# Optimization experiments

Measured on AMD Instinct MI355X. Metric: run time of the kernel, lower is better.

The kernel has to match this reference:

```python
import jax, jax.numpy as jnp
import numpy as np

N, E, DIM = 50000, 1_600_000, 96
H = DIM // 3      # num_heads = dim/3 = 32
HD = 3            # head_dim = dim/num_heads = 3
SCALE = 2.0
EPS = 1e-5


def ln(x, g, b):
    mu = x.mean(-1, keepdims=True)
    var = ((x - mu) ** 2).mean(-1, keepdims=True)
    return (x - mu) * jax.lax.rsqrt(var + EPS) * g + b


def setup_inputs() -> dict:
    key = jax.random.key(0)
    ks = jax.random.split(key, 40)
    rn = lambda k, shp, s=0.05: jax.random.normal(k, shp, jnp.float32) * s
    inp = {
        'feat': jax.random.normal(ks[0], (N, DIM), jnp.float32),
        'edge': jax.random.normal(ks[1], (E, H), jnp.float32),
        'Wq': rn(ks[2], (DIM, DIM)), 'bq': jnp.zeros((DIM,), jnp.float32),
        'Wk': rn(ks[3], (DIM, DIM)), 'bk': jnp.zeros((DIM,), jnp.float32),
        'Wv': rn(ks[4], (DIM, DIM)), 'bv': jnp.zeros((DIM,), jnp.float32),
        'We': rn(ks[5], (H, H)), 'be': jnp.zeros((H,), jnp.float32),
        'Wb': rn(ks[6], (H, H)), 'bb': jnp.zeros((H,), jnp.float32),
        'Wvv': rn(ks[7], (DIM + H, DIM)), 'bvv': jnp.zeros((DIM,), jnp.float32),
        'Wf0': rn(ks[8], (H, 2 * H)), 'bf0': jnp.zeros((2 * H,), jnp.float32),
        'Wf1': rn(ks[9], (2 * H, H)), 'bf1': jnp.zeros((H,), jnp.float32),
        'Wm0': rn(ks[10], (DIM, 2 * DIM)), 'bm0': jnp.zeros((2 * DIM,), jnp.float32),
        'Wm1': rn(ks[11], (2 * DIM, DIM)), 'bm1': jnp.zeros((DIM,), jnp.float32),
        'g_n0': jnp.ones((DIM,), jnp.float32), 'b_n0': jnp.zeros((DIM,), jnp.float32),
        'g_e0': jnp.ones((H,), jnp.float32), 'b_e0': jnp.zeros((H,), jnp.float32),
        'g_e1': jnp.ones((H,), jnp.float32), 'b_e1': jnp.zeros((H,), jnp.float32),
        'g_m': jnp.ones((DIM,), jnp.float32), 'b_m': jnp.zeros((DIM,), jnp.float32),
        'w': jnp.zeros((1,), jnp.float32),
        'src': jax.random.randint(ks[12], (E,), 0, N),
        'dst': jax.random.randint(ks[13], (E,), 0, N),
    }
    return inp


def reference(feat, edge, Wq, bq, Wk, bk, Wv, bv, We, be, Wb, bb, Wvv, bvv,
              Wf0, bf0, Wf1, bf1, Wm0, bm0, Wm1, bm1,
              g_n0, b_n0, g_e0, b_e0, g_e1, b_e1, g_m, b_m, w, src, dst):
    n = feat.shape[0]
    h0 = ln(feat, g_n0, b_n0)            # [N, DIM]
    ew = ln(edge, g_e0, b_e0)            # [E, H]
    q = (h0 @ Wq + bq).reshape(n, H, HD)
    k = (h0 @ Wk + bk).reshape(n, H, HD)
    v = (h0 @ Wv + bv).reshape(n, H, HD)
    ve = (ew @ We + be)[:, :, None]       # [E, H, 1]
    B = ew @ Wb + bb                      # [E, H]
    # src_dot_dst('k','q'): (k[src] * q[dst]).sum(-1)
    score = jnp.sum(k[src] * q[dst], axis=-1) / SCALE + B   # [E, H]
    e = score + edge                       # [E, H]
    se = jnp.concatenate([v[src], ve], axis=-1)              # [E, H, 4]
    # edge_softmax: softmax over incoming edges of each dst node, per head
    m = jax.ops.segment_max(score, dst, num_segments=n)      # [N, H]
    ex = jnp.exp(score - m[dst])
    den = jax.ops.segment_sum(ex, dst, num_segments=n)
    att = (ex / den[dst])[:, :, None]                        # [E, H, 1]
    agg = jax.ops.segment_sum(att * se, dst, num_segments=n) # [N, H, 4]
    h = feat * (1.0 + w) + (agg.reshape(n, -1) @ Wvv + bvv)  # [N, DIM]
    # up_expert Mlp (pre-LN residual)
    hn = ln(h, g_m, b_m)
    h = h + (jax.nn.relu(hn @ Wm0 + bm0) @ Wm1 + bm1)
    # edge FFN residual
    en = ln(e, g_e1, b_e1)
    e = e + (jax.nn.relu(en @ Wf0 + bf0) @ Wf1 + bf1)
    return h, e
```

## Files before the change

### kernel.cpp

```cpp
#include <hip/hip_runtime.h>
#include <cstdint>
#include <cstddef>


typedef short  s16x8 __attribute__((ext_vector_type(8)));
typedef short  s16x4 __attribute__((ext_vector_type(4)));
typedef float  f32x4 __attribute__((ext_vector_type(4)));

__device__ __forceinline__ unsigned short f2b(float x) {
    union { float f; unsigned u; } v; v.f = x;
    unsigned r = v.u + 0x7FFF + ((v.u >> 16) & 1);
    return (unsigned short)(r >> 16);
}
__device__ __forceinline__ float b2f(unsigned short u) {
    union { unsigned u; float f; } v; v.u = ((unsigned)u) << 16; return v.f;
}

template<int MULTI, int LNA, int A16, int RELU, int RES>
__global__ __launch_bounds__(256) void mgemm_kernel(
    const void* __restrict__ Av, int lda,
    const float* __restrict__ B0, const float* __restrict__ B1,
    const float* __restrict__ B2, int ldb,
    const float* __restrict__ bias0, const float* __restrict__ bias1,
    const float* __restrict__ bias2,
    const float* __restrict__ lng, const float* __restrict__ lnbv,
    const float* __restrict__ resid, const float* __restrict__ wptr,
    float* __restrict__ C, int ldc, unsigned short* __restrict__ C16,
    int M, int K)
{
    __shared__ unsigned short sAL[64 * 200];
    __shared__ unsigned short sB[96 * 40];

    const int tid = threadIdx.x;
    const int m0 = blockIdx.x * 64;
    const int y  = blockIdx.y;
    const float* B = MULTI ? (y == 0 ? B0 : (y == 1 ? B1 : B2)) : B0;
    const int nbB = MULTI ? 0 : y * 96;
    const int nbC = y * 96;
    const int w = tid >> 6, l = tid & 63, fr = l & 15, kg = l >> 4;
    const int KP = K + 8;

    if (LNA) {
        const float* Af = (const float*)Av;
        const int row = 16 * w + fr;
        const int grow = m0 + row;
        float x[24];
        if (grow < M) {
            #pragma unroll
            for (int t = 0; t < 6; t++)
                *(float4*)&x[t * 4] = *(const float4*)(Af + (size_t)grow * lda + 24 * kg + t * 4);
        } else {
            #pragma unroll
            for (int t = 0; t < 24; t++) x[t] = 0.f;
        }
        float s = 0.f;
        #pragma unroll
        for (int t = 0; t < 24; t++) s += x[t];
        s += __shfl_xor(s, 16, 64); s += __shfl_xor(s, 32, 64);
        float mu = s * (1.f / 96.f);
        float v2 = 0.f;
        #pragma unroll
        for (int t = 0; t < 24; t++) { float d = x[t] - mu; v2 += d * d; }
        v2 += __shfl_xor(v2, 16, 64); v2 += __shfl_xor(v2, 32, 64);
        float rs = rsqrtf(v2 * (1.f / 96.f) + 1e-5f);
        #pragma unroll
        for (int t3 = 0; t3 < 3; t3++) {
            s16x8 yv;
            #pragma unroll
            for (int u = 0; u < 8; u++) {
                int cidx = 24 * kg + t3 * 8 + u;
                yv[u] = (short)f2b((x[t3 * 8 + u] - mu) * rs * lng[cidx] + lnbv[cidx]);
            }
            *(s16x8*)&sAL[row * KP + 24 * kg + t3 * 8] = yv;
        }
    } else {
        const int nseg = K >> 3;
        for (int idx = tid; idx < 64 * nseg; idx += 256) {
            int row = idx / nseg, k8 = (idx - row * nseg) * 8;
            int grow = m0 + row;
            s16x8 a8 = (s16x8){0, 0, 0, 0, 0, 0, 0, 0};
            if (grow < M) {
                if (A16) {
                    a8 = *(const s16x8*)((const unsigned short*)Av + (size_t)grow * lda + k8);
                } else {
                    const float* Af = (const float*)Av;
                    float4 v0 = *(const float4*)(Af + (size_t)grow * lda + k8);
                    float4 v1 = *(const float4*)(Af + (size_t)grow * lda + k8 + 4);
                    a8[0] = (short)f2b(v0.x); a8[1] = (short)f2b(v0.y);
                    a8[2] = (short)f2b(v0.z); a8[3] = (short)f2b(v0.w);
                    a8[4] = (short)f2b(v1.x); a8[5] = (short)f2b(v1.y);
                    a8[6] = (short)f2b(v1.z); a8[7] = (short)f2b(v1.w);
                }
            }
            *(s16x8*)&sAL[row * KP + k8] = a8;
        }
    }

    f32x4 acc[6];
    #pragma unroll
    for (int i = 0; i < 6; i++) acc[i] = (f32x4){0.f, 0.f, 0.f, 0.f};

    for (int kc = 0; kc < K; kc += 32) {
        #pragma unroll
        for (int r = 0; r < 3; r++) {
            int idx = tid + 256 * r;
            int k = idx / 24, n4 = (idx - k * 24) * 4;
            float4 v = *(const float4*)(B + (size_t)(kc + k) * ldb + nbB + n4);
            sB[(n4 + 0) * 40 + k] = f2b(v.x);
            sB[(n4 + 1) * 40 + k] = f2b(v.y);
            sB[(n4 + 2) * 40 + k] = f2b(v.z);
            sB[(n4 + 3) * 40 + k] = f2b(v.w);
        }
        __syncthreads();
        {
            s16x8 a = *(s16x8*)&sAL[(16 * w + fr) * KP + kc + kg * 8];
            #pragma unroll
            for (int nt = 0; nt < 6; nt++) {
                s16x8 b = *(s16x8*)&sB[(16 * nt + fr) * 40 + kg * 8];
                acc[nt] = __builtin_amdgcn_mfma_f32_16x16x32_bf16(a, b, acc[nt], 0, 0, 0);
            }
        }
        __syncthreads();
    }

    float scale = 1.f;
    if (RES) scale = wptr ? (1.f + wptr[0]) : 1.f;
    const float* biasp = MULTI ? (y == 0 ? bias0 : (y == 1 ? bias1 : bias2)) : bias0;
    const int bbase = MULTI ? 0 : nbB;

    #pragma unroll
    for (int nt = 0; nt < 6; nt++) {
        int cl = nt * 16 + fr;
        float bv = biasp[bbase + cl];
        int gcol = nbC + cl;
        #pragma unroll
        for (int r = 0; r < 4; r++) {
            int row = m0 + 16 * w + 4 * kg + r;
            if (row >= M) continue;
            float v = acc[nt][r] + bv;
            if (RELU) v = fmaxf(v, 0.f);
            if (MULTI) {
                C16[(size_t)row * 288 + gcol] = f2b(v);
            } else {
                if (RES) v += scale * resid[(size_t)row * ldc + gcol];
                C[(size_t)row * ldc + gcol] = v;
            }
        }
    }
}

__global__ __launch_bounds__(256) void prep_kernel(
    const float* __restrict__ Wb, const float* __restrict__ We,
    const float* __restrict__ Wf0, const float* __restrict__ Wf1,
    unsigned short* __restrict__ WbWe16, unsigned short* __restrict__ Wf0T16,
    unsigned short* __restrict__ Wf1T16)
{
    const int t = threadIdx.x;
    for (int i = t; i < 2048; i += 256) {
        int n = i >> 5, k = i & 31;
        float v = (n < 32) ? Wb[k * 32 + n] : We[k * 32 + (n - 32)];
        WbWe16[i] = f2b(v);
    }
    for (int i = t; i < 2048; i += 256) {
        int n = i >> 5, k = i & 31;
        Wf0T16[i] = f2b(Wf0[k * 64 + n]);
    }
    for (int i = t; i < 2048; i += 256) {
        int n = i >> 6, k = i & 63;
        Wf1T16[i] = f2b(Wf1[k * 32 + n]);
    }
}

__global__ __launch_bounds__(256) void count_kernel(
    const int* __restrict__ dst, int* __restrict__ cnt,
    int* __restrict__ rank, int E)
{
    int i = blockIdx.x * 256 + threadIdx.x;
    if (i < E) rank[i] = atomicAdd(&cnt[dst[i]], 1);
}

__global__ __launch_bounds__(1024) void scan_kernel(
    const int* __restrict__ cnt, int* __restrict__ off, int N)
{
    __shared__ int s[1024];
    const int tid = threadIdx.x;
    const int chunk = (N + 1023) >> 10;
    const int lo = tid * chunk;
    const int hi = min(lo + chunk, N);
    int sum = 0;
    for (int i = lo; i < hi; i++) sum += cnt[i];
    s[tid] = sum;
    __syncthreads();
    for (int d = 1; d < 1024; d <<= 1) {
        int v = (tid >= d) ? s[tid - d] : 0;
        __syncthreads();
        s[tid] += v;
        __syncthreads();
    }
    int base = (tid == 0) ? 0 : s[tid - 1];
    for (int i = lo; i < hi; i++) {
        off[i] = base;
        base += cnt[i];
    }
}

__global__ __launch_bounds__(256) void scatter_kernel(
    const int* __restrict__ dst, const int* __restrict__ src,
    const int* __restrict__ off, const int* __restrict__ rank,
    int4* __restrict__ slotinfo, int E)
{
    int i = blockIdx.x * 256 + threadIdx.x;
    if (i < E) {
        int d = dst[i];
        int p = off[d] + rank[i];
        slotinfo[p] = make_int4(i, src[i], d, 0);
    }
}

__global__ __launch_bounds__(256, 5) void edge_tile_kernel(
    const float* __restrict__ edge, const unsigned short* __restrict__ qkv16,
    const int4* __restrict__ slotinfo,
    const unsigned short* __restrict__ WbWe16,
    const unsigned short* __restrict__ Wf0T16,
    const unsigned short* __restrict__ Wf1T16,
    const float* __restrict__ be, const float* __restrict__ bb,
    const float* __restrict__ bf0, const float* __restrict__ bf1,
    const float* __restrict__ ge0, const float* __restrict__ be0,
    const float* __restrict__ ge1, const float* __restrict__ be1,
    unsigned short* __restrict__ exve16, float* __restrict__ eout, int E)
{
    __shared__ float          sEV[64 * 36];
    __shared__ unsigned short sQK[64 * 44];
    __shared__ unsigned short sA [64 * 40];
    __shared__ unsigned short sX [64 * 76];

    const int tid = threadIdx.x;
    const long long e0 = (long long)blockIdx.x * 64;
    const int w  = tid >> 6;
    const int l  = tid & 63;
    const int fr = l & 15;
    const int kg = l >> 4;

    {
        const int row = tid >> 2;
        const int j   = tid & 3;
        long long s = e0 + row;
        float qv[24], kv[24];
        if (s < E) {
            int4 si = slotinfo[s];
            const unsigned short* qp = qkv16 + (size_t)si.z * 288 + 24 * j;
            const unsigned short* kp = qkv16 + (size_t)si.y * 288 + 96 + 24 * j;
            #pragma unroll
            for (int t = 0; t < 3; t++) {
                s16x8 qa = *(const s16x8*)(qp + 8 * t);
                s16x8 ka = *(const s16x8*)(kp + 8 * t);
                #pragma unroll
                for (int u = 0; u < 8; u++) {
                    qv[8 * t + u] = b2f((unsigned short)qa[u]);
                    kv[8 * t + u] = b2f((unsigned short)ka[u]);
                }
            }
        } else {
            #pragma unroll
            for (int t = 0; t < 24; t++) { qv[t] = 0.f; kv[t] = 0.f; }
        }
        s16x8 qkb;
        #pragma unroll
        for (int t = 0; t < 8; t++) {
            float d = kv[3*t]*qv[3*t] + kv[3*t+1]*qv[3*t+1] + kv[3*t+2]*qv[3*t+2];
            qkb[t] = (short)f2b(0.5f * d);
        }
        *(s16x8*)&sQK[row * 44 + 8 * j] = qkb;
    }
    #pragma unroll
    for (int rr = 0; rr < 2; rr++) {
        int idx = tid + 256 * rr;
        int row = idx >> 3, c4 = (idx & 7) * 4;
        long long s = e0 + row;
        float4 v = make_float4(0.f, 0.f, 0.f, 0.f);
        if (s < E) {
            int ge = slotinfo[s].x;
            v = *(const float4*)(edge + (size_t)ge * 32 + c4);
        }
        *(float4*)&sEV[row * 36 + c4] = v;
    }
    __syncthreads();

    {
        const int row = 16 * w + (tid & 15);
        const int q = (tid & 63) >> 4;
        float x[8];
        *(float4*)&x[0] = *(float4*)&sEV[row * 36 + 8 * q];
        *(float4*)&x[4] = *(float4*)&sEV[row * 36 + 8 * q + 4];
        float s = x[0] + x[1] + x[2] + x[3] + x[4] + x[5] + x[6] + x[7];
        s += __shfl_xor(s, 16, 64); s += __shfl_xor(s, 32, 64);
        float mu = s * (1.f / 32.f);
        float v2 = 0.f;
        #pragma unroll
        for (int i = 0; i < 8; i++) { float d = x[i] - mu; v2 += d * d; }
        v2 += __shfl_xor(v2, 16, 64); v2 += __shfl_xor(v2, 32, 64);
        float rs = rsqrtf(v2 * (1.f / 32.f) + 1e-5f);
        float4 g1 = *(const float4*)(ge0 + 8 * q), g2 = *(const float4*)(ge0 + 8 * q + 4);
        float4 b1 = *(const float4*)(be0 + 8 * q), b2 = *(const float4*)(be0 + 8 * q + 4);
        float gg[8] = {g1.x, g1.y, g1.z, g1.w, g2.x, g2.y, g2.z, g2.w};
        float bs[8] = {b1.x, b1.y, b1.z, b1.w, b2.x, b2.y, b2.z, b2.w};
        s16x8 y;
        #pragma unroll
        for (int i = 0; i < 8; i++)
            y[i] = (short)f2b((x[i] - mu) * rs * gg[i] + bs[i]);
        *(s16x8*)&sA[row * 40 + 8 * q] = y;
    }
    __builtin_amdgcn_wave_barrier();

    f32x4 acc[4];
    {
        s16x8 a = *(s16x8*)&sA[(16 * w + fr) * 40 + kg * 8];
        #pragma unroll
        for (int nt = 0; nt < 4; nt++) {
            s16x8 b = *(const s16x8*)(WbWe16 + (16 * nt + fr) * 32 + kg * 8);
            f32x4 z = {0.f, 0.f, 0.f, 0.f};
            acc[nt] = __builtin_amdgcn_mfma_f32_16x16x32_bf16(a, b, z, 0, 0, 0);
        }
    }

    #pragma unroll
    for (int nt = 0; nt < 2; nt++) {
        int col = nt * 16 + fr;
        float bbv = bb[col];
        #pragma unroll
        for (int r = 0; r < 4; r++) {
            int row = 16 * w + 4 * kg + r;
            float sc = acc[nt][r] + b2f(sQK[row * 44 + col]) + bbv;
            sX[row * 76 + col] = f2b(__expf(sc));
            float er = sc + sEV[row * 36 + col];
            sEV[row * 36 + col] = er;
        }
    }
    #pragma unroll
    for (int nt = 2; nt < 4; nt++) {
        int col = (nt - 2) * 16 + fr;
        float bev = be[col];
        #pragma unroll
        for (int r = 0; r < 4; r++) {
            int row = 16 * w + 4 * kg + r;
            sX[row * 76 + 32 + col] = f2b(acc[nt][r] + bev);
        }
    }
    __syncthreads();

    #pragma unroll
    for (int rr = 0; rr < 2; rr++) {
        int idx = tid + 256 * rr;
        int row = idx >> 3, c8 = (idx & 7) * 8;
        long long s = e0 + row;
        if (s < E)
            *(s16x8*)(exve16 + (size_t)s * 64 + c8) = *(s16x8*)&sX[row * 76 + c8];
    }
    {
        const int row = 16 * w + (tid & 15);
        const int q = (tid & 63) >> 4;
        float x[8];
        *(float4*)&x[0] = *(float4*)&sEV[row * 36 + 8 * q];
        *(float4*)&x[4] = *(float4*)&sEV[row * 36 + 8 * q + 4];
        float s = x[0] + x[1] + x[2] + x[3] + x[4] + x[5] + x[6] + x[7];
        s += __shfl_xor(s, 16, 64); s += __shfl_xor(s, 32, 64);
        float mu = s * (1.f / 32.f);
        float v2 = 0.f;
        #pragma unroll
        for (int i = 0; i < 8; i++) { float d = x[i] - mu; v2 += d * d; }
        v2 += __shfl_xor(v2, 16, 64); v2 += __shfl_xor(v2, 32, 64);
        float rs = rsqrtf(v2 * (1.f / 32.f) + 1e-5f);
        float4 g1 = *(const float4*)(ge1 + 8 * q), g2 = *(const float4*)(ge1 + 8 * q + 4);
        float4 b1 = *(const float4*)(be1 + 8 * q), b2 = *(const float4*)(be1 + 8 * q + 4);
        float gg[8] = {g1.x, g1.y, g1.z, g1.w, g2.x, g2.y, g2.z, g2.w};
        float bs[8] = {b1.x, b1.y, b1.z, b1.w, b2.x, b2.y, b2.z, b2.w};
        s16x8 y;
        #pragma unroll
        for (int i = 0; i < 8; i++)
            y[i] = (short)f2b((x[i] - mu) * rs * gg[i] + bs[i]);
        *(s16x8*)&sA[row * 40 + 8 * q] = y;
    }
    __syncthreads();

    {
        s16x8 a = *(s16x8*)&sA[(16 * w + fr) * 40 + kg * 8];
        #pragma unroll
        for (int nt = 0; nt < 4; nt++) {
            s16x8 b = *(const s16x8*)(Wf0T16 + (16 * nt + fr) * 32 + kg * 8);
            f32x4 z = {0.f, 0.f, 0.f, 0.f};
            f32x4 a2 = __builtin_amdgcn_mfma_f32_16x16x32_bf16(a, b, z, 0, 0, 0);
            int col = nt * 16 + fr;
            float b0v = bf0[col];
            #pragma unroll
            for (int r = 0; r < 4; r++) {
                int row = 16 * w + 4 * kg + r;
                sX[row * 76 + col] = f2b(fmaxf(a2[r] + b0v, 0.f));
            }
        }
    }
    __builtin_amdgcn_wave_barrier();

    {
        s16x8 a0 = *(s16x8*)&sX[(16 * w + fr) * 76 + kg * 8];
        s16x8 a1 = *(s16x8*)&sX[(16 * w + fr) * 76 + 32 + kg * 8];
        #pragma unroll
        for (int nt = 0; nt < 2; nt++) {
            s16x8 b0 = *(const s16x8*)(Wf1T16 + (16 * nt + fr) * 64 + kg * 8);
            s16x8 b1 = *(const s16x8*)(Wf1T16 + (16 * nt + fr) * 64 + 32 + kg * 8);
            f32x4 z = {0.f, 0.f, 0.f, 0.f};
            f32x4 t = __builtin_amdgcn_mfma_f32_16x16x32_bf16(a0, b0, z, 0, 0, 0);
            t = __builtin_amdgcn_mfma_f32_16x16x32_bf16(a1, b1, t, 0, 0, 0);
            int col = nt * 16 + fr;
            float bf1v = bf1[col];
            #pragma unroll
            for (int r = 0; r < 4; r++) {
                int row = 16 * w + 4 * kg + r;
                float out = t[r] + sEV[row * 36 + col] + bf1v;
                sEV[row * 36 + col] = out;
            }
        }
    }
    __syncthreads();

    #pragma unroll
    for (int rr = 0; rr < 2; rr++) {
        int idx = tid + 256 * rr;
        int row = idx >> 3, c4 = (idx & 7) * 4;
        long long s = e0 + row;
        if (s < E) {
            int ge = slotinfo[s].x;
            *(float4*)(eout + (size_t)ge * 32 + c4) = *(float4*)&sEV[row * 36 + c4];
        }
    }
}

__global__ __launch_bounds__(256) void gather_kernel(
    const unsigned short* __restrict__ exve16, const unsigned short* __restrict__ qkv16,
    const int4* __restrict__ slotinfo, const int* __restrict__ off,
    const int* __restrict__ cnt, unsigned short* __restrict__ agg16, int N)
{
    __shared__ unsigned short sV16[4][2][2][96];
    __shared__ unsigned short sE16[4][2][2][64];
    const int wave = threadIdx.x >> 6;
    const int lane = threadIdx.x & 63;
    const int head = lane & 31;
    const int half = lane >> 5;
    int n = blockIdx.x * 4 + wave;
    if (n >= N) return;
    const int o = off[n], d = cnt[n];
    float a0 = 0.f, a1 = 0.f, a2 = 0.f, a3 = 0.f, den = 0.f;
    for (int i = half; i < d; i += 4) {
        const int i2 = i + 2;
        {
            int sn = slotinfo[o + i].y;
            const unsigned short* vr = qkv16 + (size_t)sn * 288 + 192;
            const unsigned short* er = exve16 + (size_t)(o + i) * 64;
            if (head < 12)
                *(s16x8*)&sV16[wave][half][0][head * 8] = *(const s16x8*)(vr + head * 8);
            else if (head >= 24)
                *(s16x8*)&sE16[wave][half][0][(head - 24) * 8] = *(const s16x8*)(er + (head - 24) * 8);
        }
        if (i2 < d) {
            int sn = slotinfo[o + i2].y;
            const unsigned short* vr = qkv16 + (size_t)sn * 288 + 192;
            const unsigned short* er = exve16 + (size_t)(o + i2) * 64;
            if (head < 12)
                *(s16x8*)&sV16[wave][half][1][head * 8] = *(const s16x8*)(vr + head * 8);
            else if (head >= 24)
                *(s16x8*)&sE16[wave][half][1][(head - 24) * 8] = *(const s16x8*)(er + (head - 24) * 8);
        }
        __builtin_amdgcn_wave_barrier();
        {
            float ex = b2f(sE16[wave][half][0][head]);
            float vv = b2f(sE16[wave][half][0][32 + head]);
            a0 += ex * b2f(sV16[wave][half][0][head * 3]);
            a1 += ex * b2f(sV16[wave][half][0][head * 3 + 1]);
            a2 += ex * b2f(sV16[wave][half][0][head * 3 + 2]);
            a3 += ex * vv;
            den += ex;
        }
        if (i2 < d) {
            float ex = b2f(sE16[wave][half][1][head]);
            float vv = b2f(sE16[wave][half][1][32 + head]);
            a0 += ex * b2f(sV16[wave][half][1][head * 3]);
            a1 += ex * b2f(sV16[wave][half][1][head * 3 + 1]);
            a2 += ex * b2f(sV16[wave][half][1][head * 3 + 2]);
            a3 += ex * vv;
            den += ex;
        }
        __builtin_amdgcn_wave_barrier();
    }
    a0 += __shfl_xor(a0, 32, 64);
    a1 += __shfl_xor(a1, 32, 64);
    a2 += __shfl_xor(a2, 32, 64);
    a3 += __shfl_xor(a3, 32, 64);
    den += __shfl_xor(den, 32, 64);
    if (half == 0) {
        float sc = (d > 0) ? 1.f / den : 0.f;
        s16x4 ov;
        ov[0] = (short)f2b(a0 * sc);
        ov[1] = (short)f2b(a1 * sc);
        ov[2] = (short)f2b(a2 * sc);
        ov[3] = (short)f2b(a3 * sc);
        *(s16x4*)(agg16 + (size_t)n * 128 + head * 4) = ov;
    }
}

extern "C" void kernel_launch(void* const* d_in, const int* in_sizes, int n_in,
                              void* d_out, int out_size, void* d_ws, size_t ws_size,
                              hipStream_t stream)
{
    (void)n_in; (void)out_size; (void)ws_size;
    const float* feat = (const float*)d_in[0];
    const float* edge = (const float*)d_in[1];
    const float* Wq   = (const float*)d_in[2];
    const float* bq   = (const float*)d_in[3];
    const float* Wk   = (const float*)d_in[4];
    const float* bk   = (const float*)d_in[5];
    const float* Wv   = (const float*)d_in[6];
    const float* bv   = (const float*)d_in[7];
    const float* We   = (const float*)d_in[8];
    const float* be   = (const float*)d_in[9];
    const float* Wb   = (const float*)d_in[10];
    const float* bb   = (const float*)d_in[11];
    const float* Wvv  = (const float*)d_in[12];
    const float* bvv  = (const float*)d_in[13];
    const float* Wf0  = (const float*)d_in[14];
    const float* bf0  = (const float*)d_in[15];
    const float* Wf1  = (const float*)d_in[16];
    const float* bf1  = (const float*)d_in[17];
    const float* Wm0  = (const float*)d_in[18];
    const float* bm0  = (const float*)d_in[19];
    const float* Wm1  = (const float*)d_in[20];
    const float* bm1  = (const float*)d_in[21];
    const float* g_n0 = (const float*)d_in[22];
    const float* b_n0 = (const float*)d_in[23];
    const float* g_e0 = (const float*)d_in[24];
    const float* b_e0 = (const float*)d_in[25];
    const float* g_e1 = (const float*)d_in[26];
    const float* b_e1 = (const float*)d_in[27];
    const float* g_m  = (const float*)d_in[28];
    const float* b_m  = (const float*)d_in[29];
    const float* wsc  = (const float*)d_in[30];
    const int*   src  = (const int*)d_in[31];
    const int*   dst  = (const int*)d_in[32];

    const int N = in_sizes[0] / 96;
    const int E = in_sizes[1] / 32;

    float* ws    = (float*)d_ws;
    float* hp    = ws;
    float* tbuf  = hp + (size_t)N * 96;
    unsigned short* agg16 = (unsigned short*)(tbuf + (size_t)N * 192);
    unsigned short* qkv16 = agg16 + (size_t)N * 128;
    unsigned short* exve16 = qkv16 + (size_t)N * 288;
    unsigned short* wbwe16 = exve16 + (size_t)E * 64;
    unsigned short* wf0t16 = wbwe16 + 2048;
    unsigned short* wf1t16 = wf0t16 + 2048;
    int4*  slotinfo = (int4*)(wf1t16 + 2048);
    int*   rank  = (int*)(slotinfo + E);
    int*   cnt   = rank + E;
    int*   offv  = cnt + N;
    float* hout  = (float*)d_out;
    float* eoutp = (float*)d_out + (size_t)N * 96;

    hipMemsetAsync(cnt, 0, (size_t)N * sizeof(int), stream);

    const int mt = (N + 63) / 64;
    const int et = (E + 255) / 256;

    prep_kernel<<<1, 256, 0, stream>>>(Wb, We, Wf0, Wf1, wbwe16, wf0t16, wf1t16);
    count_kernel<<<et, 256, 0, stream>>>(dst, cnt, rank, E);
    scan_kernel<<<1, 1024, 0, stream>>>(cnt, offv, N);
    scatter_kernel<<<et, 256, 0, stream>>>(dst, src, offv, rank, slotinfo, E);

    mgemm_kernel<1,1,0,0,0><<<dim3(mt, 3), 256, 0, stream>>>(
        feat, 96, Wq, Wk, Wv, 96, bq, bk, bv, g_n0, b_n0,
        nullptr, nullptr, nullptr, 0, qkv16, N, 96);

    edge_tile_kernel<<<(E + 63) / 64, 256, 0, stream>>>(edge, qkv16, slotinfo,
                                             wbwe16, wf0t16, wf1t16,
                                             be, bb, bf0, bf1,
                                             g_e0, b_e0, g_e1, b_e1,
                                             exve16, eoutp, E);

    gather_kernel<<<(N + 3) / 4, 256, 0, stream>>>(exve16, qkv16, slotinfo, offv, cnt, agg16, N);

    mgemm_kernel<0,0,1,0,1><<<dim3(mt, 1), 256, 0, stream>>>(
        agg16, 128, Wvv, Wvv, Wvv, 96, bvv, bvv, bvv, nullptr, nullptr,
        feat, wsc, hp, 96, nullptr, N, 128);
    mgemm_kernel<0,1,0,1,0><<<dim3(mt, 2), 256, 0, stream>>>(
        hp, 96, Wm0, Wm0, Wm0, 192, bm0, bm0, bm0, g_m, b_m,
        nullptr, nullptr, tbuf, 192, nullptr, N, 96);
    mgemm_kernel<0,0,0,0,1><<<dim3(mt, 1), 256, 0, stream>>>(
        tbuf, 192, Wm1, Wm1, Wm1, 96, bm1, bm1, bm1, nullptr, nullptr,
        hp, nullptr, hout, 96, nullptr, N, 192);
}
```

Measured before the change: 783.9 us.

## Fuse Wvv projection, LayerNorm and two-layer MLP into one node kernel

Replaces three separate GEMM launches (Wvv projection with residual, LN+Wm0+ReLU, Wm1 with residual) with a single mlp_kernel that keeps the intermediate h and hidden activations in shared memory per 64-row tile. Weights are pre-transposed to bf16 once in prep_kernel and read directly from global/L2 instead of being staged and converted each k-step. This removes the hp and tbuf round trips through global memory and two launches. The cost is a large shared-memory footprint per block (about 60 KB), which may limit occupancy, and the single-block prep kernel now does more serial conversion work. The RES path in mgemm is also removed as dead code.

Result: no change. 795.1 us (+1.4%).

```diff
diff --git a/kernel.cpp b/kernel.cpp
--- a/kernel.cpp
+++ b/kernel.cpp
@@ -123,8 +123,6 @@
         __syncthreads();
     }
 
-    float scale = 1.f;
-    if (RES) scale = wptr ? (1.f + wptr[0]) : 1.f;
     const float* biasp = MULTI ? (y == 0 ? bias0 : (y == 1 ? bias1 : bias2)) : bias0;
     const int bbase = MULTI ? 0 : nbB;
 
@@ -142,7 +140,6 @@
             if (MULTI) {
                 C16[(size_t)row * 288 + gcol] = f2b(v);
             } else {
-                if (RES) v += scale * resid[(size_t)row * ldc + gcol];
                 C[(size_t)row * ldc + gcol] = v;
             }
         }
@@ -152,8 +149,11 @@
 __global__ __launch_bounds__(256) void prep_kernel(
     const float* __restrict__ Wb, const float* __restrict__ We,
     const float* __restrict__ Wf0, const float* __restrict__ Wf1,
+    const float* __restrict__ Wvv, const float* __restrict__ Wm0,
+    const float* __restrict__ Wm1,
     unsigned short* __restrict__ WbWe16, unsigned short* __restrict__ Wf0T16,
-    unsigned short* __restrict__ Wf1T16)
+    unsigned short* __restrict__ Wf1T16, unsigned short* __restrict__ WvvT16,
+    unsigned short* __restrict__ Wm0T16, unsigned short* __restrict__ Wm1T16)
 {
     const int t = threadIdx.x;
     for (int i = t; i < 2048; i += 256) {
@@ -168,6 +168,18 @@
     for (int i = t; i < 2048; i += 256) {
         int n = i >> 6, k = i & 63;
         Wf1T16[i] = f2b(Wf1[k * 32 + n]);
+    }
+    for (int i = t; i < 12288; i += 256) {
+        int n = i >> 7, k = i & 127;
+        WvvT16[i] = f2b(Wvv[k * 96 + n]);
+    }
+    for (int i = t; i < 18432; i += 256) {
+        int n = i / 96, k = i - n * 96;
+        Wm0T16[i] = f2b(Wm0[k * 192 + n]);
+    }
+    for (int i = t; i < 18432; i += 256) {
+        int n = i / 192, k = i - n * 192;
+        Wm1T16[i] = f2b(Wm1[k * 96 + n]);
     }
 }
 
@@ -503,6 +515,149 @@
         ov[2] = (short)f2b(a2 * sc);
         ov[3] = (short)f2b(a3 * sc);
         *(s16x4*)(agg16 + (size_t)n * 128 + head * 4) = ov;
+    }
+}
+
+__global__ __launch_bounds__(256, 2) void mlp_kernel(
+    const unsigned short* __restrict__ agg16, const float* __restrict__ feat,
+    const unsigned short* __restrict__ WvvT16,
+    const unsigned short* __restrict__ Wm0T16,
+    const unsigned short* __restrict__ Wm1T16,
+    const float* __restrict__ bvv, const float* __restrict__ bm0,
+    const float* __restrict__ bm1,
+    const float* __restrict__ g_m, const float* __restrict__ b_m,
+    const float* __restrict__ wsc,
+    float* __restrict__ hout, int M)
+{
+    __shared__ unsigned short sU[64 * 200];
+    __shared__ float          sHP[64 * 100];
+    __shared__ unsigned short sA[64 * 104];
+
+    const int tid = threadIdx.x;
+    const int m0 = blockIdx.x * 64;
+    const int w = tid >> 6, l = tid & 63, fr = l & 15, kg = l >> 4;
+
+    #pragma unroll
+    for (int r = 0; r < 4; r++) {
+        int s1 = tid + 256 * r;
+        int row = s1 >> 4, k8 = (s1 & 15) * 8;
+        int grow = m0 + row;
+        s16x8 a8 = (s16x8){0, 0, 0, 0, 0, 0, 0, 0};
+        if (grow < M) a8 = *(const s16x8*)(agg16 + (size_t)grow * 128 + k8);
+        *(s16x8*)&sU[row * 136 + k8] = a8;
+    }
+    __syncthreads();
+    const float w0 = 1.f + wsc[0];
+
+    {
+        f32x4 acc[6];
+        #pragma unroll
+        for (int i = 0; i < 6; i++) acc[i] = (f32x4){0.f, 0.f, 0.f, 0.f};
+        #pragma unroll
+        for (int kc = 0; kc < 128; kc += 32) {
+            s16x8 a = *(s16x8*)&sU[(16 * w + fr) * 136 + kc + kg * 8];
+            #pragma unroll
+            for (int nt = 0; nt < 6; nt++) {
+                s16x8 b = *(const s16x8*)(WvvT16 + (16 * nt + fr) * 128 + kc + kg * 8);
+                acc[nt] = __builtin_amdgcn_mfma_f32_16x16x32_bf16(a, b, acc[nt], 0, 0, 0);
+            }
+        }
+        #pragma unroll
+        for (int nt = 0; nt < 6; nt++) {
+            int col = nt * 16 + fr;
+            float bv = bvv[col];
+            #pragma unroll
+            for (int r = 0; r < 4; r++) {
+                int row = 16 * w + 4 * kg + r;
+                int grow = m0 + row;
+                float fv = (grow < M) ? feat[(size_t)grow * 96 + col] : 0.f;
+                sHP[row * 100 + col] = acc[nt][r] + bv + w0 * fv;
+            }
+        }
+    }
+    __syncthreads();
+
+    {
+        const int row = 16 * w + (tid & 15);
+        const int q = (tid & 63) >> 4;
+        float x[24];
+        #pragma unroll
+        for (int t = 0; t < 6; t++)
+            *(float4*)&x[t * 4] = *(float4*)&sHP[row * 100 + 24 * q + t * 4];
+        float s = 0.f;
+        #pragma unroll
+        for (int t = 0; t < 24; t++) s += x[t];
+        s += __shfl_xor(s, 16, 64); s += __shfl_xor(s, 32, 64);
+        float mu = s * (1.f / 96.f);
+        float v2 = 0.f;
+        #pragma unroll
+        for (int t = 0; t < 24; t++) { float d = x[t] - mu; v2 += d * d; }
+        v2 += __shfl_xor(v2, 16, 64); v2 += __shfl_xor(v2, 32, 64);
+        float rs = rsqrtf(v2 * (1.f / 96.f) + 1e-5f);
+        #pragma unroll
+        for (int t3 = 0; t3 < 3; t3++) {
+            s16x8 yv;
+            #pragma unroll
+            for (int u = 0; u < 8; u++) {
+                int cidx = 24 * q + t3 * 8 + u;
+                yv[u] = (short)f2b((x[t3 * 8 + u] - mu) * rs * g_m[cidx] + b_m[cidx]);
+            }
+            *(s16x8*)&sA[row * 104 + 24 * q + t3 * 8] = yv;
+        }
+    }
+    __builtin_amdgcn_wave_barrier();
+
+    {
+        f32x4 acc2[12];
+        #pragma unroll
+        for (int i = 0; i < 12; i++) acc2[i] = (f32x4){0.f, 0.f, 0.f, 0.f};
+        #pragma unroll
+        for (int kc = 0; kc < 96; kc += 32) {
+            s16x8 a = *(s16x8*)&sA[(16 * w + fr) * 104 + kc + kg * 8];
+            #pragma unroll
+            for (int nt = 0; nt < 12; nt++) {
+                s16x8 b = *(const s16x8*)(Wm0T16 + (16 * nt + fr) * 96 + kc + kg * 8);
+                acc2[nt] = __builtin_amdgcn_mfma_f32_16x16x32_bf16(a, b, acc2[nt], 0, 0, 0);
+            }
+        }
+        #pragma unroll
+        for (int nt = 0; nt < 12; nt++) {
+            int col = nt * 16 + fr;
+            float b0 = bm0[col];
+            #pragma unroll
+            for (int r = 0; r < 4; r++) {
+                int row = 16 * w + 4 * kg + r;
+                sU[row * 200 + col] = f2b(fmaxf(acc2[nt][r] + b0, 0.f));
+            }
+        }
+    }
+    __builtin_amdgcn_wave_barrier();
+
+    {
+        f32x4 acc3[6];
+        #pragma unroll
+        for (int i = 0; i < 6; i++) acc3[i] = (f32x4){0.f, 0.f, 0.f, 0.f};
+        #pragma unroll
+        for (int kc = 0; kc < 192; kc += 32) {
+            s16x8 a = *(s16x8*)&sU[(16 * w + fr) * 200 + kc + kg * 8];
+            #pragma unroll
+            for (int nt = 0; nt < 6; nt++) {
+                s16x8 b = *(const s16x8*)(Wm1T16 + (16 * nt + fr) * 192 + kc + kg * 8);
+                acc3[nt] = __builtin_amdgcn_mfma_f32_16x16x32_bf16(a, b, acc3[nt], 0, 0, 0);
+            }
+        }
+        #pragma unroll
+        for (int nt = 0; nt < 6; nt++) {
+            int col = nt * 16 + fr;
+            float bv = bm1[col];
+            #pragma unroll
+            for (int r = 0; r < 4; r++) {
+                int row = 16 * w + 4 * kg + r;
+                int grow = m0 + row;
+                if (grow < M)
+                    hout[(size_t)grow * 96 + col] = acc3[nt][r] + bv + sHP[row * 100 + col];
+            }
+        }
     }
 }
 
@@ -548,16 +703,16 @@
     const int N = in_sizes[0] / 96;
     const int E = in_sizes[1] / 32;
 
-    float* ws    = (float*)d_ws;
-    float* hp    = ws;
-    float* tbuf  = hp + (size_t)N * 96;
-    unsigned short* agg16 = (unsigned short*)(tbuf + (size_t)N * 192);
+    unsigned short* agg16 = (unsigned short*)d_ws;
     unsigned short* qkv16 = agg16 + (size_t)N * 128;
     unsigned short* exve16 = qkv16 + (size_t)N * 288;
     unsigned short* wbwe16 = exve16 + (size_t)E * 64;
     unsigned short* wf0t16 = wbwe16 + 2048;
     unsigned short* wf1t16 = wf0t16 + 2048;
-    int4*  slotinfo = (int4*)(wf1t16 + 2048);
+    unsigned short* wvvt16 = wf1t16 + 2048;
+    unsigned short* wm0t16 = wvvt16 + 12288;
+    unsigned short* wm1t16 = wm0t16 + 18432;
+    int4*  slotinfo = (int4*)(((uintptr_t)(wm1t16 + 18432) + 15) & ~(uintptr_t)15);
     int*   rank  = (int*)(slotinfo + E);
     int*   cnt   = rank + E;
     int*   offv  = cnt + N;
@@ -569,7 +724,8 @@
     const int mt = (N + 63) / 64;
     const int et = (E + 255) / 256;
 
-    prep_kernel<<<1, 256, 0, stream>>>(Wb, We, Wf0, Wf1, wbwe16, wf0t16, wf1t16);
+    prep_kernel<<<1, 256, 0, stream>>>(Wb, We, Wf0, Wf1, Wvv, Wm0, Wm1,
+                                       wbwe16, wf0t16, wf1t16, wvvt16, wm0t16, wm1t16);
     count_kernel<<<et, 256, 0, stream>>>(dst, cnt, rank, E);
     scan_kernel<<<1, 1024, 0, stream>>>(cnt, offv, N);
     scatter_kernel<<<et, 256, 0, stream>>>(dst, src, offv, rank, slotinfo, E);
@@ -586,13 +742,6 @@
 
     gather_kernel<<<(N + 3) / 4, 256, 0, stream>>>(exve16, qkv16, slotinfo, offv, cnt, agg16, N);
 
-    mgemm_kernel<0,0,1,0,1><<<dim3(mt, 1), 256, 0, stream>>>(
-        agg16, 128, Wvv, Wvv, Wvv, 96, bvv, bvv, bvv, nullptr, nullptr,
-        feat, wsc, hp, 96, nullptr, N, 128);
-    mgemm_kernel<0,1,0,1,0><<<dim3(mt, 2), 256, 0, stream>>>(
-        hp, 96, Wm0, Wm0, Wm0, 192, bm0, bm0, bm0, g_m, b_m,
-        nullptr, nullptr, tbuf, 192, nullptr, N, 96);
-    mgemm_kernel<0,0,0,0,1><<<dim3(mt, 1), 256, 0, stream>>>(
-        tbuf, 192, Wm1, Wm1, Wm1, 96, bm1, bm1, bm1, nullptr, nullptr,
-        hp, nullptr, hout, 96, nullptr, N, 192);
-}
+    mlp_kernel<<<mt, 256, 0, stream>>>(agg16, feat, wvvt16, wm0t16, wm1t16,
+                                       bvv, bm0, bm1, g_m, b_m, wsc, hout, N);
+}
```
